# Kernel optimization log

Measured on AMD Instinct MI355X. Metric: run time of the kernel, lower is better.

The kernel has to match this reference:

```python
import jax, jax.numpy as jnp
import numpy as np

N_NODES = 100000
N_EDGES = 1600000
IN_F = 128
HID = 128
OUT = 2


def setup_inputs() -> dict:
    key = jax.random.key(0)
    ks = jax.random.split(key, 12)
    s = lambda k, sh, f: jax.random.normal(k, sh, dtype=jnp.float32) * (1.0 / np.sqrt(f))
    return {
        "x": jax.random.normal(ks[0], (N_NODES, IN_F), dtype=jnp.float32),
        "W_self1": s(ks[1], (IN_F, HID), IN_F),
        "W_neigh1": s(ks[2], (IN_F, HID), IN_F),
        "b1": jnp.zeros((HID,), dtype=jnp.float32),
        "W_self2": s(ks[3], (HID, HID), HID),
        "W_neigh2": s(ks[4], (HID, HID), HID),
        "b2": jnp.zeros((HID,), dtype=jnp.float32),
        "W_final": s(ks[5], (HID, OUT), HID),
        "b_final": jnp.zeros((OUT,), dtype=jnp.float32),
        "src": jax.random.randint(ks[6], (N_EDGES,), 0, N_NODES, dtype=jnp.int32),
        "dst": jax.random.randint(ks[7], (N_EDGES,), 0, N_NODES, dtype=jnp.int32),
    }


def _sage_mean(x, src, dst, n_nodes, W_self, W_neigh, b):
    # gather neighbor (src) features, scatter-mean onto dst nodes
    msg_sum = jax.ops.segment_sum(x[src], dst, num_segments=n_nodes)  # [N, F]
    deg = jax.ops.segment_sum(jnp.ones((src.shape[0],), x.dtype), dst,
                              num_segments=n_nodes)  # [N]
    h_neigh = msg_sum / jnp.maximum(deg, 1.0)[:, None]
    # DGL SAGEConv(mean): fc_self(h_self) + fc_neigh(h_neigh) (+ bias)
    return x @ W_self + h_neigh @ W_neigh + b


def reference(x, W_self1, W_neigh1, b1, W_self2, W_neigh2, b2,
              W_final, b_final, src, dst):
    n = x.shape[0]
    h = jax.nn.relu(_sage_mean(x, src, dst, n, W_self1, W_neigh1, b1))
    h = jax.nn.relu(_sage_mean(h, src, dst, n, W_self2, W_neigh2, b2))
    return h @ W_final + b_final  # [N, 2]
```

## Files before the change

kernel.cpp:

```cpp
#include <hip/hip_runtime.h>

#define N_NODES 100000
#define N_EDGES 1600000
#define F 128

#define BSHIFT 9
#define BNODES 512
#define NBUCK 196
#define P1_BLOCKS 128
#define P1_TPB 256
#define EPB1 (N_EDGES / P1_BLOCKS)
#define CAPB 160
#define SRC_SHIFT 12
#define NSPLIT 25
#define KEYS (BNODES * NSPLIT)
#define P2_TPB 512

typedef _Float16 f16x8 __attribute__((ext_vector_type(8)));
typedef _Float16 f16x4 __attribute__((ext_vector_type(4)));
typedef _Float16 f16x2 __attribute__((ext_vector_type(2)));
typedef float f32x4 __attribute__((ext_vector_type(4)));

__global__ __launch_bounds__(P1_TPB) void k_part(const int* __restrict__ src,
                                                 const int* __restrict__ dst,
                                                 int* __restrict__ stage,
                                                 int* __restrict__ pcnt) {
    __shared__ int cnt[NBUCK];
    int t = threadIdx.x, blk = blockIdx.x;
    if (t < NBUCK) cnt[t] = 0;
    __syncthreads();
    int base = blk * EPB1;
    for (int i = t; i < EPB1; i += P1_TPB) {
        int e = base + i;
        int s = src[e], d = dst[e];
        int b = d >> BSHIFT;
        int pos = atomicAdd(&cnt[b], 1);
        if (pos < CAPB)
            stage[((long)b * P1_BLOCKS + blk) * CAPB + pos] = (s << BSHIFT) | (d & (BNODES - 1));
    }
    __syncthreads();
    if (t < NBUCK) pcnt[t * P1_BLOCKS + blk] = min(cnt[t], CAPB);
}

__global__ void k_bucketsum(const int* __restrict__ pcnt, int* __restrict__ bbase,
                            int* __restrict__ row_start) {
    __shared__ int tot[NBUCK];
    int t = threadIdx.x;
    for (int b = t; b < NBUCK; b += 256) {
        int s = 0;
        for (int i = 0; i < P1_BLOCKS; i++) s += pcnt[b * P1_BLOCKS + i];
        tot[b] = s;
    }
    __syncthreads();
    if (t == 0) {
        int acc = 0;
        for (int i = 0; i < NBUCK; i++) {
            bbase[i] = acc;
            acc += tot[i];
        }
        bbase[NBUCK] = acc;
        row_start[N_NODES] = acc;
    }
}

__global__ __launch_bounds__(P2_TPB) void k_build(const int* __restrict__ stage,
                                                  const int* __restrict__ pcnt,
                                                  const int* __restrict__ bbase,
                                                  int* __restrict__ row_start,
                                                  int* __restrict__ esrc) {
    __shared__ int cnt[KEYS];
    __shared__ int scanw[P2_TPB / 64];
    int b = blockIdx.x, t = threadIdx.x;
    int nodeBase = b * BNODES;
    for (int i = t; i < KEYS; i += P2_TPB) cnt[i] = 0;
    __syncthreads();
    int grp = t >> 7, gt = t & 127;
    for (int s = grp; s < P1_BLOCKS; s += 4) {
        int n = pcnt[b * P1_BLOCKS + s];
        const int* seg = &stage[((long)b * P1_BLOCKS + s) * CAPB];
        for (int i = gt; i < n; i += 128) {
            int pk = seg[i];
            atomicAdd(&cnt[(pk & (BNODES - 1)) * NSPLIT + (pk >> (BSHIFT + SRC_SHIFT))], 1);
        }
    }
    __syncthreads();
    int kbase = t * 25;
    int sum = 0;
#pragma unroll
    for (int i = 0; i < 25; i++) sum += cnt[kbase + i];
    int lane = t & 63, wv = t >> 6;
    int x = sum;
#pragma unroll
    for (int off = 1; off < 64; off <<= 1) {
        int y = __shfl_up(x, off, 64);
        if (lane >= off) x += y;
    }
    if (lane == 63) scanw[wv] = x;
    __syncthreads();
    if (t == 0) {
        int acc = 0;
        for (int i = 0; i < P2_TPB / 64; i++) {
            int y = scanw[i];
            scanw[i] = acc;
            acc += y;
        }
    }
    __syncthreads();
    int run = x - sum + scanw[wv];
#pragma unroll
    for (int i = 0; i < 25; i++) {
        int c = cnt[kbase + i];
        cnt[kbase + i] = run;
        run += c;
    }
    __syncthreads();
    int base0 = bbase[b];
    {
        int node = nodeBase + t;
        if (t < BNODES && node < N_NODES) row_start[node] = base0 + cnt[t * NSPLIT];
    }
    __syncthreads();
    for (int s = grp; s < P1_BLOCKS; s += 4) {
        int n = pcnt[b * P1_BLOCKS + s];
        const int* seg = &stage[((long)b * P1_BLOCKS + s) * CAPB];
        for (int i = gt; i < n; i += 128) {
            int pk = seg[i];
            int pos = atomicAdd(&cnt[(pk & (BNODES - 1)) * NSPLIT + (pk >> (BSHIFT + SRC_SHIFT))], 1);
            esrc[base0 + pos] = pk >> BSHIFT;
        }
    }
}

__global__ void k_cast(const float* __restrict__ x, _Float16* __restrict__ xh, int n4) {
    int i = blockIdx.x * blockDim.x + threadIdx.x;
    if (i < n4) {
        float4 v = ((const float4*)x)[i];
        f16x4 h;
        h.x = (_Float16)v.x; h.y = (_Float16)v.y;
        h.z = (_Float16)v.z; h.w = (_Float16)v.w;
        ((f16x4*)xh)[i] = h;
    }
}

__global__ void k_prepw(const float* __restrict__ Ws1, const float* __restrict__ Wn1,
                        const float* __restrict__ Ws2, const float* __restrict__ Wn2,
                        _Float16* __restrict__ Wt1, _Float16* __restrict__ Wt2) {
    int i = blockIdx.x * blockDim.x + threadIdx.x;
    int which = i >> 15;
    int j = i & 32767;
    int n = j >> 8;
    int k = j & 255;
    const float* Ws = which ? Ws2 : Ws1;
    const float* Wn = which ? Wn2 : Wn1;
    _Float16* Wt = which ? Wt2 : Wt1;
    float v = (k < 128) ? Ws[k * F + n] : Wn[(k - 128) * F + n];
    Wt[n * 256 + k] = (_Float16)v;
}

__global__ __launch_bounds__(256) void k_agg(const f16x2* __restrict__ xf,
                                             const int* __restrict__ row_start,
                                             const int* __restrict__ esrc,
                                             f16x2* __restrict__ out) {
    int wave = (int)((blockIdx.x * blockDim.x + threadIdx.x) >> 6);
    int lane = threadIdx.x & 63;
    if (wave >= N_NODES) return;
    int beg = row_start[wave], end = row_start[wave + 1];
    int deg = end - beg;
    int e = 0;
    if (lane < deg) e = esrc[beg + lane];
    float ax = 0.f, ay = 0.f;
    int n64 = min(deg, 64);
    int i = 0;
    for (; i + 8 <= n64; i += 8) {
        int s0 = __shfl(e, i + 0, 64);
        int s1 = __shfl(e, i + 1, 64);
        int s2 = __shfl(e, i + 2, 64);
        int s3 = __shfl(e, i + 3, 64);
        int s4 = __shfl(e, i + 4, 64);
        int s5 = __shfl(e, i + 5, 64);
        int s6 = __shfl(e, i + 6, 64);
        int s7 = __shfl(e, i + 7, 64);
        f16x2 v0 = xf[(long)s0 * 64 + lane];
        f16x2 v1 = xf[(long)s1 * 64 + lane];
        f16x2 v2 = xf[(long)s2 * 64 + lane];
        f16x2 v3 = xf[(long)s3 * 64 + lane];
        f16x2 v4 = xf[(long)s4 * 64 + lane];
        f16x2 v5 = xf[(long)s5 * 64 + lane];
        f16x2 v6 = xf[(long)s6 * 64 + lane];
        f16x2 v7 = xf[(long)s7 * 64 + lane];
        ax += ((float)v0.x + (float)v1.x) + ((float)v2.x + (float)v3.x) +
              ((float)v4.x + (float)v5.x) + ((float)v6.x + (float)v7.x);
        ay += ((float)v0.y + (float)v1.y) + ((float)v2.y + (float)v3.y) +
              ((float)v4.y + (float)v5.y) + ((float)v6.y + (float)v7.y);
    }
    for (; i + 2 <= n64; i += 2) {
        int s0 = __shfl(e, i + 0, 64);
        int s1 = __shfl(e, i + 1, 64);
        f16x2 v0 = xf[(long)s0 * 64 + lane];
        f16x2 v1 = xf[(long)s1 * 64 + lane];
        ax += (float)v0.x + (float)v1.x;
        ay += (float)v0.y + (float)v1.y;
    }
    for (; i < n64; i++) {
        int s = __shfl(e, i, 64);
        f16x2 v = xf[(long)s * 64 + lane];
        ax += (float)v.x;
        ay += (float)v.y;
    }
    for (int j = beg + 64; j < end; j++) {
        int s = esrc[j];
        f16x2 v = xf[(long)s * 64 + lane];
        ax += (float)v.x;
        ay += (float)v.y;
    }
    float inv = (deg > 0) ? 1.0f / (float)deg : 0.0f;
    f16x2 r;
    r.x = (_Float16)(ax * inv);
    r.y = (_Float16)(ay * inv);
    out[(long)wave * 64 + lane] = r;
}

template <bool FINAL>
__global__ __launch_bounds__(256, 2) void k_gemm_mfma(
    const _Float16* __restrict__ Aself, const _Float16* __restrict__ Aneigh,
    const _Float16* __restrict__ Wt, const float* __restrict__ bias,
    _Float16* __restrict__ Hout, const float* __restrict__ Wf,
    const float* __restrict__ bf, float* __restrict__ Out) {
    const int M = N_NODES;
    __shared__ _Float16 Wl[4096 * 8];
    int w = threadIdx.x >> 6;
    int lane = threadIdx.x & 63;
    int q = lane >> 4;
    int ln = lane & 15;
    int rBase = blockIdx.x * 128 + w * 32;

#pragma unroll
    for (int i = 0; i < 16; i++) {
        int s = threadIdx.x + i * 256;
        int L = s & 63, ct = (s >> 6) & 7, ks = s >> 9;
        int g = (ct * 16 + (L & 15)) * 256 + ks * 32 + (L >> 4) * 8;
        *(f16x8*)&Wl[s * 8] = *(const f16x8*)&Wt[g];
    }

    f32x4 acc[2][8];
#pragma unroll
    for (int rt = 0; rt < 2; rt++)
#pragma unroll
        for (int ct = 0; ct < 8; ct++) acc[rt][ct] = (f32x4){0.f, 0.f, 0.f, 0.f};

    __syncthreads();

    for (int ks = 0; ks < 8; ks++) {
        const _Float16* Abase = (ks < 4) ? Aself : Aneigh;
        int k0 = (ks & 3) * 32;
        f16x8 b[8];
#pragma unroll
        for (int ct = 0; ct < 8; ct++)
            b[ct] = *(const f16x8*)&Wl[((ks * 8 + ct) * 64 + lane) * 8];
#pragma unroll
        for (int rt = 0; rt < 2; rt++) {
            int row = rBase + rt * 16 + ln;
            f16x8 a = {};
            if (row < M) a = *(const f16x8*)&Abase[(long)row * F + k0 + q * 8];
#pragma unroll
            for (int ct = 0; ct < 8; ct++)
                acc[rt][ct] = __builtin_amdgcn_mfma_f32_16x16x32_f16(a, b[ct], acc[rt][ct], 0, 0, 0);
        }
    }

    float bv[8];
#pragma unroll
    for (int ct = 0; ct < 8; ct++) bv[ct] = bias[ct * 16 + ln];

    if (!FINAL) {
#pragma unroll
        for (int rt = 0; rt < 2; rt++) {
#pragma unroll
            for (int r = 0; r < 4; r++) {
                int row = rBase + rt * 16 + q * 4 + r;
                if (row < M) {
#pragma unroll
                    for (int ct = 0; ct < 8; ct++) {
                        float h = acc[rt][ct][r] + bv[ct];
                        h = h > 0.f ? h : 0.f;
                        Hout[(long)row * F + ct * 16 + ln] = (_Float16)h;
                    }
                }
            }
        }
    } else {
        float wf0[8], wf1[8];
#pragma unroll
        for (int ct = 0; ct < 8; ct++) {
            int c = ct * 16 + ln;
            wf0[ct] = Wf[c * 2 + 0];
            wf1[ct] = Wf[c * 2 + 1];
        }
        float bf0 = bf[0], bf1 = bf[1];
#pragma unroll
        for (int rt = 0; rt < 2; rt++) {
#pragma unroll
            for (int r = 0; r < 4; r++) {
                int row = rBase + rt * 16 + q * 4 + r;
                float p0 = 0.f, p1 = 0.f;
#pragma unroll
                for (int ct = 0; ct < 8; ct++) {
                    float h = acc[rt][ct][r] + bv[ct];
                    h = h > 0.f ? h : 0.f;
                    p0 += h * wf0[ct];
                    p1 += h * wf1[ct];
                }
#pragma unroll
                for (int off = 1; off < 16; off <<= 1) {
                    p0 += __shfl_xor(p0, off, 64);
                    p1 += __shfl_xor(p1, off, 64);
                }
                if (ln == 0 && row < M) {
                    Out[(long)row * 2 + 0] = p0 + bf0;
                    Out[(long)row * 2 + 1] = p1 + bf1;
                }
            }
        }
    }
}

extern "C" void kernel_launch(void* const* d_in, const int* in_sizes, int n_in,
                              void* d_out, int out_size, void* d_ws, size_t ws_size,
                              hipStream_t stream) {
    const float* x   = (const float*)d_in[0];
    const float* Ws1 = (const float*)d_in[1];
    const float* Wn1 = (const float*)d_in[2];
    const float* b1  = (const float*)d_in[3];
    const float* Ws2 = (const float*)d_in[4];
    const float* Wn2 = (const float*)d_in[5];
    const float* b2  = (const float*)d_in[6];
    const float* Wf  = (const float*)d_in[7];
    const float* bf  = (const float*)d_in[8];
    const int* src   = (const int*)d_in[9];
    const int* dst   = (const int*)d_in[10];
    float* out = (float*)d_out;

    char* ws = (char*)d_ws;
    int*      row_start = (int*)(ws + 0);
    int*      bbase     = (int*)(ws + 400016);
    int*      pcnt      = (int*)(ws + 400816);
    int*      stage     = (int*)(ws + 501184);
    int*      esrc      = (int*)(ws + 16557504);
    _Float16* xh        = (_Float16*)(ws + 22957504);
    _Float16* hneigh    = (_Float16*)(ws + 48557504);
    _Float16* h1        = (_Float16*)(ws + 74157504);
    _Float16* Wt1       = (_Float16*)(ws + 99757504);
    _Float16* Wt2       = (_Float16*)(ws + 99823040);

    const int TPB = 256;
    k_part<<<P1_BLOCKS, P1_TPB, 0, stream>>>(src, dst, stage, pcnt);
    k_bucketsum<<<1, 256, 0, stream>>>(pcnt, bbase, row_start);
    k_build<<<NBUCK, P2_TPB, 0, stream>>>(stage, pcnt, bbase, row_start, esrc);

    k_cast<<<(N_NODES * F / 4 + TPB - 1) / TPB, TPB, 0, stream>>>(x, xh, N_NODES * F / 4);
    k_prepw<<<256, 256, 0, stream>>>(Ws1, Wn1, Ws2, Wn2, Wt1, Wt2);

    k_agg<<<(N_NODES + 3) / 4, 256, 0, stream>>>((const f16x2*)xh, row_start, esrc,
                                                 (f16x2*)hneigh);
    k_gemm_mfma<false><<<(N_NODES + 127) / 128, 256, 0, stream>>>(
        xh, hneigh, Wt1, b1, h1, nullptr, nullptr, nullptr);
    k_agg<<<(N_NODES + 3) / 4, 256, 0, stream>>>((const f16x2*)h1, row_start, esrc,
                                                 (f16x2*)hneigh);
    k_gemm_mfma<true><<<(N_NODES + 127) / 128, 256, 0, stream>>>(
        h1, hneigh, Wt2, b2, nullptr, Wf, bf, out);
}
```

Measured before the change: 385.1 us.

## Store features in column-chunked planes and aggregate one chunk per block

Features move from row-major [N,128] fp16 to 8 planes of [N,16] fp16, one per 16-column chunk. Cast, aggregation and GEMM kernels now all read and write this layout. The aggregation kernel now works on a single plane per block, with 8 lane groups each gathering 32-byte rows for different edges, followed by a cross-group shuffle reduction. The goal is to keep each plane's gather working set small enough to stay cache-resident and to improve L2 locality. The cost is that every edge index is read 8 times, and reads become 32-byte segments instead of 256-byte rows.

New measurement: 684.9 us. 77.8% more time.

```diff
diff --git a/kernel.cpp b/kernel.cpp
--- a/kernel.cpp
+++ b/kernel.cpp
@@ -131,15 +131,16 @@
     }
 }
 
-__global__ void k_cast(const float* __restrict__ x, _Float16* __restrict__ xh, int n4) {
+__global__ void k_cast(const float* __restrict__ x, _Float16* __restrict__ xc) {
     int i = blockIdx.x * blockDim.x + threadIdx.x;
-    if (i < n4) {
-        float4 v = ((const float4*)x)[i];
-        f16x4 h;
-        h.x = (_Float16)v.x; h.y = (_Float16)v.y;
-        h.z = (_Float16)v.z; h.w = (_Float16)v.w;
-        ((f16x4*)xh)[i] = h;
-    }
+    int node = i >> 3, c = i & 7;
+    const float* xp = &x[(long)node * F + c * 16];
+    _Float16 h[16];
+#pragma unroll
+    for (int j = 0; j < 16; j++) h[j] = (_Float16)xp[j];
+    _Float16* op = &xc[((long)c * N_NODES + node) * 16];
+    *(f16x8*)op = *(f16x8*)&h[0];
+    *(f16x8*)(op + 8) = *(f16x8*)&h[8];
 }
 
 __global__ void k_prepw(const float* __restrict__ Ws1, const float* __restrict__ Wn1,
@@ -157,67 +158,52 @@
     Wt[n * 256 + k] = (_Float16)v;
 }
 
-__global__ __launch_bounds__(256) void k_agg(const f16x2* __restrict__ xf,
+__global__ __launch_bounds__(256) void k_agg(const f16x2* __restrict__ xc,
                                              const int* __restrict__ row_start,
                                              const int* __restrict__ esrc,
-                                             f16x2* __restrict__ out) {
-    int wave = (int)((blockIdx.x * blockDim.x + threadIdx.x) >> 6);
+                                             f16x2* __restrict__ outc) {
+    int c = blockIdx.x & 7;
+    int nb = blockIdx.x >> 3;
+    int w = threadIdx.x >> 6;
     int lane = threadIdx.x & 63;
-    if (wave >= N_NODES) return;
-    int beg = row_start[wave], end = row_start[wave + 1];
+    int node = nb * 4 + w;
+    int grp = lane >> 3;
+    int col = lane & 7;
+    int beg = row_start[node], end = row_start[node + 1];
     int deg = end - beg;
+    int n64 = min(deg, 64);
     int e = 0;
-    if (lane < deg) e = esrc[beg + lane];
+    if (lane < n64) e = __builtin_nontemporal_load(&esrc[beg + lane]);
+    const f16x2* plane = xc + (long)c * (N_NODES * 8);
     float ax = 0.f, ay = 0.f;
-    int n64 = min(deg, 64);
-    int i = 0;
-    for (; i + 8 <= n64; i += 8) {
-        int s0 = __shfl(e, i + 0, 64);
-        int s1 = __shfl(e, i + 1, 64);
-        int s2 = __shfl(e, i + 2, 64);
-        int s3 = __shfl(e, i + 3, 64);
-        int s4 = __shfl(e, i + 4, 64);
-        int s5 = __shfl(e, i + 5, 64);
-        int s6 = __shfl(e, i + 6, 64);
-        int s7 = __shfl(e, i + 7, 64);
-        f16x2 v0 = xf[(long)s0 * 64 + lane];
-        f16x2 v1 = xf[(long)s1 * 64 + lane];
-        f16x2 v2 = xf[(long)s2 * 64 + lane];
-        f16x2 v3 = xf[(long)s3 * 64 + lane];
-        f16x2 v4 = xf[(long)s4 * 64 + lane];
-        f16x2 v5 = xf[(long)s5 * 64 + lane];
-        f16x2 v6 = xf[(long)s6 * 64 + lane];
-        f16x2 v7 = xf[(long)s7 * 64 + lane];
-        ax += ((float)v0.x + (float)v1.x) + ((float)v2.x + (float)v3.x) +
-              ((float)v4.x + (float)v5.x) + ((float)v6.x + (float)v7.x);
-        ay += ((float)v0.y + (float)v1.y) + ((float)v2.y + (float)v3.y) +
-              ((float)v4.y + (float)v5.y) + ((float)v6.y + (float)v7.y);
-    }
-    for (; i + 2 <= n64; i += 2) {
-        int s0 = __shfl(e, i + 0, 64);
-        int s1 = __shfl(e, i + 1, 64);
-        f16x2 v0 = xf[(long)s0 * 64 + lane];
-        f16x2 v1 = xf[(long)s1 * 64 + lane];
-        ax += (float)v0.x + (float)v1.x;
-        ay += (float)v0.y + (float)v1.y;
-    }
-    for (; i < n64; i++) {
-        int s = __shfl(e, i, 64);
-        f16x2 v = xf[(long)s * 64 + lane];
+    for (int i = 0; i < n64; i += 16) {
+        int i0 = i + grp, i1 = i + 8 + grp;
+        int s0 = __shfl(e, i0, 64);
+        int s1 = __shfl(e, i1, 64);
+        f16x2 v0 = plane[(long)s0 * 8 + col];
+        f16x2 v1 = plane[(long)s1 * 8 + col];
+        if (i0 < n64) { ax += (float)v0.x; ay += (float)v0.y; }
+        if (i1 < n64) { ax += (float)v1.x; ay += (float)v1.y; }
+    }
+    for (int j = beg + 64 + grp; j < end; j += 8) {
+        int s = __builtin_nontemporal_load(&esrc[j]);
+        f16x2 v = plane[(long)s * 8 + col];
         ax += (float)v.x;
         ay += (float)v.y;
     }
-    for (int j = beg + 64; j < end; j++) {
-        int s = esrc[j];
-        f16x2 v = xf[(long)s * 64 + lane];
-        ax += (float)v.x;
-        ay += (float)v.y;
-    }
-    float inv = (deg > 0) ? 1.0f / (float)deg : 0.0f;
-    f16x2 r;
-    r.x = (_Float16)(ax * inv);
-    r.y = (_Float16)(ay * inv);
-    out[(long)wave * 64 + lane] = r;
+    ax += __shfl_xor(ax, 8, 64);
+    ay += __shfl_xor(ay, 8, 64);
+    ax += __shfl_xor(ax, 16, 64);
+    ay += __shfl_xor(ay, 16, 64);
+    ax += __shfl_xor(ax, 32, 64);
+    ay += __shfl_xor(ay, 32, 64);
+    if (grp == 0) {
+        float inv = (deg > 0) ? 1.0f / (float)deg : 0.0f;
+        f16x2 r;
+        r.x = (_Float16)(ax * inv);
+        r.y = (_Float16)(ay * inv);
+        __builtin_nontemporal_store(r, &outc[(long)c * (N_NODES * 8) + (long)node * 8 + col]);
+    }
 }
 
 template <bool FINAL>
@@ -252,7 +238,9 @@
 
     for (int ks = 0; ks < 8; ks++) {
         const _Float16* Abase = (ks < 4) ? Aself : Aneigh;
-        int k0 = (ks & 3) * 32;
+        int kk = (ks & 3) * 32 + q * 8;
+        int chk = kk >> 4;
+        int inner = kk & 15;
         f16x8 b[8];
 #pragma unroll
         for (int ct = 0; ct < 8; ct++)
@@ -261,7 +249,7 @@
         for (int rt = 0; rt < 2; rt++) {
             int row = rBase + rt * 16 + ln;
             f16x8 a = {};
-            if (row < M) a = *(const f16x8*)&Abase[(long)row * F + k0 + q * 8];
+            if (row < M) a = *(const f16x8*)&Abase[((long)chk * N_NODES + row) * 16 + inner];
 #pragma unroll
             for (int ct = 0; ct < 8; ct++)
                 acc[rt][ct] = __builtin_amdgcn_mfma_f32_16x16x32_f16(a, b[ct], acc[rt][ct], 0, 0, 0);
@@ -283,7 +271,7 @@
                     for (int ct = 0; ct < 8; ct++) {
                         float h = acc[rt][ct][r] + bv[ct];
                         h = h > 0.f ? h : 0.f;
-                        Hout[(long)row * F + ct * 16 + ln] = (_Float16)h;
+                        Hout[((long)ct * N_NODES + row) * 16 + ln] = (_Float16)h;
                     }
                 }
             }
@@ -352,20 +340,17 @@
     _Float16* Wt1       = (_Float16*)(ws + 99757504);
     _Float16* Wt2       = (_Float16*)(ws + 99823040);
 
-    const int TPB = 256;
     k_part<<<P1_BLOCKS, P1_TPB, 0, stream>>>(src, dst, stage, pcnt);
     k_bucketsum<<<1, 256, 0, stream>>>(pcnt, bbase, row_start);
     k_build<<<NBUCK, P2_TPB, 0, stream>>>(stage, pcnt, bbase, row_start, esrc);
 
-    k_cast<<<(N_NODES * F / 4 + TPB - 1) / TPB, TPB, 0, stream>>>(x, xh, N_NODES * F / 4);
+    k_cast<<<3125, 256, 0, stream>>>(x, xh);
     k_prepw<<<256, 256, 0, stream>>>(Ws1, Wn1, Ws2, Wn2, Wt1, Wt2);
 
-    k_agg<<<(N_NODES + 3) / 4, 256, 0, stream>>>((const f16x2*)xh, row_start, esrc,
-                                                 (f16x2*)hneigh);
+    k_agg<<<200000, 256, 0, stream>>>((const f16x2*)xh, row_start, esrc, (f16x2*)hneigh);
     k_gemm_mfma<false><<<(N_NODES + 127) / 128, 256, 0, stream>>>(
         xh, hneigh, Wt1, b1, h1, nullptr, nullptr, nullptr);
-    k_agg<<<(N_NODES + 3) / 4, 256, 0, stream>>>((const f16x2*)h1, row_start, esrc,
-                                                 (f16x2*)hneigh);
+    k_agg<<<200000, 256, 0, stream>>>((const f16x2*)h1, row_start, esrc, (f16x2*)hneigh);
     k_gemm_mfma<true><<<(N_NODES + 127) / 128, 256, 0, stream>>>(
         h1, hneigh, Wt2, b2, nullptr, Wf, bf, out);
 }
```
